# Optimization experiments

Hardware: AMD Instinct MI355X
Metric: run time of the kernel (lower is better)

## Reference

```python
import jax, jax.numpy as jnp
import numpy as np

N, E = 50000, 250000
SD, VM = 128, 64          # scalar channels, vector multiplicity (irreps: 128x0e + 64x1e)
EA, SH = 64, 4            # edge_attr dim, spherical-harmonics dim (1x0e + 1x1e)
H, FC = 16, 256
HD = FC // H              # head dim = 16
EPS = 1e-5


def _split(x):
    return x[:, :SD], x[:, SD:].reshape(-1, VM, 3)


def _ln(s, V):
    # equivariant layer norm: standardize scalars; RMS-normalize vector norms
    s = (s - s.mean(-1, keepdims=True)) * jax.lax.rsqrt(s.var(-1, keepdims=True) + EPS)
    vn = jax.lax.rsqrt(jnp.mean(jnp.sum(V * V, -1), -1, keepdims=True) + EPS)
    return s, V * vn[..., None]


def setup_inputs() -> dict:
    key = jax.random.key(0)
    ks = iter(jax.random.split(key, 48))
    rn = lambda shp, sc=1.0: jax.random.normal(next(ks), shp, dtype=jnp.float32) * sc
    w = lambda i, o: rn((i, o), 1.0 / np.sqrt(i))
    z = lambda d: jnp.zeros((d,), jnp.float32)
    return dict(
        node_features=rn((N, SD + 3 * VM)),
        edge_attr=rn((E, EA)),
        edge_sh=rn((E, SH)),
        Wq=w(SD, FC), bq=z(FC),
        Wk=w(SD, FC), bk=z(FC),
        We=w(EA, FC), be=z(FC),
        Wv_s=w(SD, SD), bv_s=z(SD), Wv_v=w(VM, VM),
        w_ss=w(SD, SD), w_vv_s=w(VM, SD), w_ssg=w(SD, VM), w_vvg=w(VM, VM),
        b_ms=z(SD), b_mg=z(VM),
        w_sv=w(SD, VM), w_vs=w(VM, VM), w_vvv=w(VM, VM),
        Wo_s=w(SD, SD), bo_s=z(SD), Wo_v=w(VM, VM),
        W1_s=w(SD, SD + VM), b1_s=z(SD + VM), W1_v=w(VM, VM),
        W2_s=w(SD, SD), b2_s=z(SD), W2_v=w(VM, VM),
        edge_index=jax.random.randint(next(ks), (2, E), 0, N, dtype=jnp.int32),
        batch=jnp.zeros((N,), jnp.int32),
    )


def reference(node_features, edge_attr, edge_sh, Wq, bq, Wk, bk, We, be,
              Wv_s, bv_s, Wv_v, w_ss, w_vv_s, w_ssg, w_vvg, b_ms, b_mg,
              w_sv, w_vs, w_vvv, Wo_s, bo_s, Wo_v,
              W1_s, b1_s, W1_v, W2_s, b2_s, W2_v, edge_index, batch):
    src, dst = edge_index[0], edge_index[1]
    ns, nV = _split(node_features)                        # [N,SD], [N,VM,3]

    # per-edge multi-head attention scores (gathered q/k + edge bias term)
    q = (ns[dst] @ Wq + bq).reshape(-1, H, HD)
    k = (ns[src] @ Wk + bk).reshape(-1, H, HD)
    ef = (edge_attr @ We + be).reshape(-1, H, HD)
    scores = ((q * k).sum(-1) + (q * ef).sum(-1)) / np.sqrt(HD)   # [E,H]

    # per-destination-node softmax (replaces the python unique(dst) loop)
    m = jax.ops.segment_max(scores, dst, num_segments=N)
    ex = jnp.exp(scores - m[dst])
    den = jax.ops.segment_sum(ex, dst, num_segments=N)
    attn = (ex / den[dst]).mean(-1, keepdims=True)                # [E,1]

    # v projection (o3.Linear) on source nodes
    vs = ns[src] @ Wv_s + bv_s                                    # [E,SD]
    Vv = jnp.einsum('evk,vu->euk', nV[src], Wv_v)                 # [E,VM,3]

    # message MLP: fully-connected tensor product with edge SH, norm, swish-gate
    shs, shv = edge_sh[:, 0], edge_sh[:, 1:4]
    s_in = vs * shs[:, None]                                      # 0e x 0e -> 0e
    dots = jnp.einsum('evk,ek->ev', Vv, shv)                      # 1e x 1e -> 0e
    ms = s_in @ w_ss + dots @ w_vv_s + b_ms                       # [E,SD] scalars
    mg = s_in @ w_ssg + dots @ w_vvg + b_mg                       # [E,VM] gates
    MV = ((vs @ w_sv)[:, :, None] * shv[:, None, :]               # 0e x 1e -> 1e
          + jnp.einsum('evk,vu->euk', Vv * shs[:, None, None], w_vs)   # 1e x 0e -> 1e
          + jnp.einsum('evk,vu->euk', jnp.cross(Vv, shv[:, None, :]), w_vvv))  # 1e x 1e -> 1e
    sg, MVn = _ln(jnp.concatenate([ms, mg], -1), MV)
    msg_s = jax.nn.silu(sg[:, :SD])
    msg_V = MVn * jax.nn.sigmoid(sg[:, SD:])[:, :, None]

    # attention-weighted scatter-sum aggregation to destination nodes
    agg_s = jax.ops.segment_sum(msg_s * attn, dst, num_segments=N)
    agg_V = jax.ops.segment_sum(msg_V * attn[:, :, None], dst, num_segments=N)

    # out projection + residual + norm1
    x_s = ns + (agg_s @ Wo_s + bo_s)
    x_V = nV + jnp.einsum('nvk,vu->nuk', agg_V, Wo_v)
    x_s, x_V = _ln(x_s, x_V)

    # gated equivariant FFN + residual + norm2
    f = x_s @ W1_s + b1_s                                         # [N,SD+VM]
    fV = jnp.einsum('nvk,vu->nuk', x_V, W1_v)
    gV = fV * jax.nn.sigmoid(f[:, SD:])[:, :, None]
    o_s = x_s + (jax.nn.silu(f[:, :SD]) @ W2_s + b2_s)
    o_V = x_V + jnp.einsum('nvk,vu->nuk', gV, W2_v)
    o_s, o_V = _ln(o_s, o_V)
    return jnp.concatenate([o_s, o_V.reshape(-1, 3 * VM)], -1)
```

## Files before the change

kernel.cpp:

```cpp
#include <hip/hip_runtime.h>
#include <hip/hip_bf16.h>

#define NNODE 50000
#define NEDGE 250000

typedef __hip_bfloat16 bf16;
typedef __attribute__((ext_vector_type(8))) short short8v;
typedef __attribute__((ext_vector_type(4))) float f32x4;

__device__ __forceinline__ float b2f(bf16 x){ return __bfloat162float(x); }
__device__ __forceinline__ bf16  f2b(float x){ return __float2bfloat16(x); }
__device__ __forceinline__ short f2s(float x){ bf16 h=f2b(x); short s; __builtin_memcpy(&s,&h,2); return s; }
__device__ __forceinline__ float s2f(short s){ bf16 h; __builtin_memcpy(&h,&s,2); return b2f(h); }
__device__ __forceinline__ float sigm(float x){ return 1.0f/(1.0f+__expf(-x)); }
__device__ __forceinline__ float wred64(float v){
  #pragma unroll
  for(int o=32;o>0;o>>=1) v+=__shfl_xor(v,o,64);
  return v;
}
__device__ __forceinline__ float gred16(float v){
  v+=__shfl_xor(v,1,64); v+=__shfl_xor(v,2,64); v+=__shfl_xor(v,4,64); v+=__shfl_xor(v,8,64);
  return v;
}
__device__ __forceinline__ int ired64(int v){
  #pragma unroll
  for(int o=32;o>0;o>>=1) v+=__shfl_xor(v,o,64);
  return v;
}
__device__ __forceinline__ int fragOff(int r, int k){
  int kt=k>>5, k32=k&31, half=k32>>4, g=(k32&15)>>2, j=k32&3;
  return (kt<<10)+((r+(g<<4))<<4)+(half<<3)+(j<<1);
}
__device__ __forceinline__ short8v pack8(float4 a, float4 b){
  short8v s; s[0]=f2s(a.x);s[1]=f2s(a.y);s[2]=f2s(a.z);s[3]=f2s(a.w);
  s[4]=f2s(b.x);s[5]=f2s(b.y);s[6]=f2s(b.z);s[7]=f2s(b.w); return s;
}
__device__ __forceinline__ short8v pack8s(short4 a, short4 b){
  short8v s; s[0]=a.x;s[1]=a.y;s[2]=a.z;s[3]=a.w;s[4]=b.x;s[5]=b.y;s[6]=b.z;s[7]=b.w; return s;
}

#define T_WOS 0
#define T_WOV 32
#define T_W1S 40
#define T_W1V 88
#define T_W2S 96
#define T_W2V 128
#define T_WE  136
#define T_WQ  168
#define T_WK  232
#define T_WVS 296
#define T_WSS 328
#define T_WSSG 360
#define T_WSV 376
#define T_WVV 392
#define T_WVVS 400
#define T_WVVG 416
#define T_WVS2 424
#define T_WVVV 432
#define T_TOT 440

__global__ __launch_bounds__(64) void k_prep(
  const float* __restrict__ Wo_s, const float* __restrict__ Wo_v,
  const float* __restrict__ W1_s, const float* __restrict__ W1_v,
  const float* __restrict__ W2_s, const float* __restrict__ W2_v,
  const float* __restrict__ WeM,
  const float* __restrict__ Wq, const float* __restrict__ Wk,
  const float* __restrict__ Wv_s,
  const float* __restrict__ w_ss, const float* __restrict__ w_ssg,
  const float* __restrict__ w_sv,
  const float* __restrict__ Wv_v, const float* __restrict__ w_vv_s,
  const float* __restrict__ w_vvg, const float* __restrict__ w_vs,
  const float* __restrict__ w_vvv,
  short* __restrict__ P)
{
  const int T=blockIdx.x, l=threadIdx.x;
  const float* W; int N, KT, lt;
  if(T<T_WOV){ W=Wo_s; N=128; KT=4; lt=T; }
  else if(T<T_W1S){ W=Wo_v; N=64; KT=2; lt=T-T_WOV; }
  else if(T<T_W1V){ W=W1_s; N=192; KT=4; lt=T-T_W1S; }
  else if(T<T_W2S){ W=W1_v; N=64; KT=2; lt=T-T_W1V; }
  else if(T<T_W2V){ W=W2_s; N=128; KT=4; lt=T-T_W2S; }
  else if(T<T_WE){ W=W2_v; N=64; KT=2; lt=T-T_W2V; }
  else if(T<T_WQ){ W=WeM; N=256; KT=2; lt=T-T_WE; }
  else if(T<T_WK){ W=Wq; N=256; KT=4; lt=T-T_WQ; }
  else if(T<T_WVS){ W=Wk; N=256; KT=4; lt=T-T_WK; }
  else if(T<T_WSS){ W=Wv_s; N=128; KT=4; lt=T-T_WVS; }
  else if(T<T_WSSG){ W=w_ss; N=128; KT=4; lt=T-T_WSS; }
  else if(T<T_WSV){ W=w_ssg; N=64; KT=4; lt=T-T_WSSG; }
  else if(T<T_WVV){ W=w_sv; N=64; KT=4; lt=T-T_WSV; }
  else if(T<T_WVVS){ W=Wv_v; N=64; KT=2; lt=T-T_WVV; }
  else if(T<T_WVVG){ W=w_vv_s; N=128; KT=2; lt=T-T_WVVS; }
  else if(T<T_WVS2){ W=w_vvg; N=64; KT=2; lt=T-T_WVVG; }
  else if(T<T_WVVV){ W=w_vs; N=64; KT=2; lt=T-T_WVS2; }
  else { W=w_vvv; N=64; KT=2; lt=T-T_WVVV; }
  const int nt=lt/KT, kt=lt-nt*KT;
  const int col=nt*16+(l&15);
  short8v o;
  #pragma unroll
  for(int j=0;j<8;j++){
    int k=kt*32+((j>>2)<<4)+((l>>4)<<2)+(j&3);
    o[j]=f2s(W[(size_t)k*N+col]);
  }
  *(short8v*)(P+((size_t)T<<9)+(l<<3))=o;
}


__global__ __launch_bounds__(256) void k1_mfma(
  const float* __restrict__ nf, const short* __restrict__ P,
  const float* __restrict__ bq, const float* __restrict__ bk,
  const float* __restrict__ bvs,
  bf16* __restrict__ Q, bf16* __restrict__ K, short* __restrict__ NREC2)
{
  __shared__ __align__(16) short nsF[4*512];
  __shared__ __align__(16) short vsF[4*512];
  const int t=threadIdx.x, l=t&63, w=t>>6;
  const int n0=blockIdx.x*16;
  for(int i=t;i<512;i+=256){
    int r=i>>5, c=(i&31)<<2;
    const float4 v=*(const float4*)&nf[(size_t)(n0+r)*320+c];
    short4 s; s.x=f2s(v.x); s.y=f2s(v.y); s.z=f2s(v.z); s.w=f2s(v.w);
    *(short4*)((char*)nsF+fragOff(r,c))=s;
  }
  __syncthreads();
  short8v a[4];
  #pragma unroll
  for(int kt=0;kt<4;kt++) a[kt]=*(const short8v*)((const char*)nsF+(kt<<10)+(l<<4));
  #pragma unroll
  for(int ii=0;ii<4;ii++){
    int nt=w+(ii<<2);
    f32x4 accq={0.f,0.f,0.f,0.f}, acck={0.f,0.f,0.f,0.f};
    #pragma unroll
    for(int kt=0;kt<4;kt++){
      short8v bq8=*(const short8v*)(P+(((size_t)(T_WQ+nt*4+kt))<<9)+(l<<3));
      short8v bk8=*(const short8v*)(P+(((size_t)(T_WK+nt*4+kt))<<9)+(l<<3));
      accq=__builtin_amdgcn_mfma_f32_16x16x32_bf16(a[kt],bq8,accq,0,0,0);
      acck=__builtin_amdgcn_mfma_f32_16x16x32_bf16(a[kt],bk8,acck,0,0,0);
    }
    int col=(nt<<4)+(l&15);
    float bqs=bq[col], bks=bk[col];
    #pragma unroll
    for(int r=0;r<4;r++){
      int row=((l>>4)<<2)+r;
      Q[(size_t)(n0+row)*256+col]=f2b(accq[r]+bqs);
      K[(size_t)(n0+row)*256+col]=f2b(acck[r]+bks);
    }
  }
  #pragma unroll
  for(int ii=0;ii<2;ii++){
    int nt=w+(ii<<2);
    f32x4 acc={0.f,0.f,0.f,0.f};
    #pragma unroll
    for(int kt=0;kt<4;kt++){
      short8v b=*(const short8v*)(P+(((size_t)(T_WVS+nt*4+kt))<<9)+(l<<3));
      acc=__builtin_amdgcn_mfma_f32_16x16x32_bf16(a[kt],b,acc,0,0,0);
    }
    int col=(nt<<4)+(l&15);
    float bv=bvs[col];
    #pragma unroll
    for(int r=0;r<4;r++){
      int row=((l>>4)<<2)+r;
      *(short*)((char*)vsF+fragOff(row,col))=f2s(acc[r]+bv);
    }
  }
  __syncthreads();
  #pragma unroll
  for(int kt=0;kt<4;kt++) a[kt]=*(const short8v*)((const char*)vsF+(kt<<10)+(l<<4));
  #pragma unroll
  for(int ii=0;ii<4;ii++){
    int nt=w+(ii<<2);
    int bt;
    if(nt<8) bt=T_WSS+nt*4;
    else if(nt<12) bt=T_WSSG+(nt-8)*4;
    else bt=T_WSV+(nt-12)*4;
    f32x4 acc={0.f,0.f,0.f,0.f};
    #pragma unroll
    for(int kt=0;kt<4;kt++){
      short8v b=*(const short8v*)(P+(((size_t)(bt+kt))<<9)+(l<<3));
      acc=__builtin_amdgcn_mfma_f32_16x16x32_bf16(a[kt],b,acc,0,0,0);
    }
    int col=(nt<<4)+(l&15);
    int lane, sslot;
    if(nt<8){ lane=col&63; sslot=(col>=64)?1:0; }
    else if(nt<12){ lane=col-128; sslot=2; }
    else { lane=col-192; sslot=3; }
    #pragma unroll
    for(int r=0;r<4;r++){
      int row=((l>>4)<<2)+r;
      NREC2[(size_t)(n0+row)*1280 + (lane<<2) + sslot]=f2s(acc[r]);
    }
  }
}

__global__ __launch_bounds__(256) void k2_mfma(
  const float* __restrict__ nf, const short* __restrict__ P,
  short* __restrict__ NREC2)
{
  __shared__ __align__(16) short nvF[6*512];
  __shared__ __align__(16) short vvF[6*512];
  const int t=threadIdx.x, l=t&63, w=t>>6;
  const int n0=blockIdx.x*16;
  for(int i=t;i<3072;i+=256){
    int r=i/192, c=i-r*192;
    int v=c/3, k=c-3*v;
    float x=nf[(size_t)(n0+r)*320+128+c];
    *(short*)((char*)nvF+(k<<11)+fragOff(r,v))=f2s(x);
  }
  __syncthreads();
  #pragma unroll
  for(int jj=0;jj<3;jj++){
    int job=w+(jj<<2);
    int p=job>>2, nt=job&3;
    f32x4 acc={0.f,0.f,0.f,0.f};
    #pragma unroll
    for(int kt=0;kt<2;kt++){
      short8v a2=*(const short8v*)((const char*)nvF+(p<<11)+(kt<<10)+(l<<4));
      short8v b=*(const short8v*)(P+(((size_t)(T_WVV+nt*2+kt))<<9)+(l<<3));
      acc=__builtin_amdgcn_mfma_f32_16x16x32_bf16(a2,b,acc,0,0,0);
    }
    int col=(nt<<4)+(l&15);
    #pragma unroll
    for(int r=0;r<4;r++){
      int row=((l>>4)<<2)+r;
      *(short*)((char*)vvF+(p<<11)+fragOff(row,col))=f2s(acc[r]);
    }
  }
  __syncthreads();
  #pragma unroll
  for(int jj=0;jj<15;jj++){
    int job=w+(jj<<2);
    int p=job/20, r20=job-p*20;
    int nt, bt, G0;
    if(r20<8){ nt=r20; bt=T_WVVS+nt*2; G0=0; }
    else if(r20<12){ nt=r20-8; bt=T_WVVG+nt*2; G0=1; }
    else if(r20<16){ nt=r20-12; bt=T_WVS2+nt*2; G0=2; }
    else { nt=r20-16; bt=T_WVVV+nt*2; G0=3; }
    f32x4 acc={0.f,0.f,0.f,0.f};
    #pragma unroll
    for(int kt=0;kt<2;kt++){
      short8v a2=*(const short8v*)((const char*)vvF+(p<<11)+(kt<<10)+(l<<4));
      short8v b=*(const short8v*)(P+(((size_t)(bt+kt))<<9)+(l<<3));
      acc=__builtin_amdgcn_mfma_f32_16x16x32_bf16(a2,b,acc,0,0,0);
    }
    int col=(nt<<4)+(l&15);
    int G;
    if(G0==0)      G = p*2 + (col>=64 ? 1 : 0);
    else if(G0==1) G = 6 + p;
    else if(G0==2) G = 9 + p;
    else           G = 12 + p;
    int lane = col & 63;
    int addr = ((1+(G>>2))<<8) + (lane<<2) + (G&3);
    #pragma unroll
    for(int r=0;r<4;r++){
      int row=((l>>4)<<2)+r;
      NREC2[(size_t)(n0+row)*1280 + addr]=f2s(acc[r]);
    }
  }
}

#define SCAN_NB 196

__global__ __launch_bounds__(256) void k_scan1(const int* __restrict__ counts, int* __restrict__ bsum){
  const int t=threadIdx.x, ln=t&63, wid=t>>6;
  int idx=blockIdx.x*256+t;
  int v=(idx<NNODE)?counts[idx]:0;
  int s=ired64(v);
  __shared__ int ws[4];
  if(ln==0) ws[wid]=s;
  __syncthreads();
  if(t==0) bsum[blockIdx.x]=ws[0]+ws[1]+ws[2]+ws[3];
}

__global__ __launch_bounds__(256) void k_scan2(const int* __restrict__ bsum, int* __restrict__ boff){
  const int t=threadIdx.x, ln=t&63, wid=t>>6;
  int v=(t<SCAN_NB)?bsum[t]:0;
  int incl=v;
  #pragma unroll
  for(int o=1;o<64;o<<=1){ int x=__shfl_up(incl,o,64); if(ln>=o) incl+=x; }
  __shared__ int wtot[4], wpre[4];
  if(ln==63) wtot[wid]=incl;
  __syncthreads();
  if(t==0){ int s=0; for(int k=0;k<4;k++){ wpre[k]=s; s+=wtot[k]; } }
  __syncthreads();
  if(t<SCAN_NB) boff[t]=wpre[wid]+incl-v;
}

__global__ __launch_bounds__(256) void k_scan3(const int* __restrict__ counts, const int* __restrict__ boff,
                                               int* __restrict__ off, int* __restrict__ cursor){
  const int t=threadIdx.x, ln=t&63, wid=t>>6;
  int idx=blockIdx.x*256+t;
  int v=(idx<NNODE)?counts[idx]:0;
  int incl=v;
  #pragma unroll
  for(int o=1;o<64;o<<=1){ int x=__shfl_up(incl,o,64); if(ln>=o) incl+=x; }
  __shared__ int wtot[4], wpre[4];
  if(ln==63) wtot[wid]=incl;
  __syncthreads();
  if(t==0){ int s=0; for(int k=0;k<4;k++){ wpre[k]=s; s+=wtot[k]; } }
  __syncthreads();
  int excl=boff[blockIdx.x]+wpre[wid]+incl-v;
  if(idx<NNODE){ off[idx]=excl; cursor[idx]=excl; }
  if(blockIdx.x==SCAN_NB-1 && t==255) off[NNODE]=NEDGE;
}

__global__ __launch_bounds__(256) void k_scatter(
  const int* __restrict__ eidx, const float* __restrict__ esh,
  int* __restrict__ cursor, int* __restrict__ eord,
  int* __restrict__ srcs, float* __restrict__ eshs)
{
  int e=blockIdx.x*256+threadIdx.x;
  if(e<NEDGE){
    int d=eidx[NEDGE+e];
    int pos=atomicAdd(&cursor[d],1);
    eord[pos]=e;
    srcs[pos]=eidx[e];
    *(float4*)&eshs[(size_t)pos*4]=*(const float4*)&esh[(size_t)e*4];
  }
}

__global__ __launch_bounds__(256) void k3_mfma(
  const float* __restrict__ eattr, const int* __restrict__ eidx,
  const short* __restrict__ P, const float* __restrict__ be,
  const bf16* __restrict__ Q, const bf16* __restrict__ K,
  float* __restrict__ SC, int* __restrict__ counts)
{
  __shared__ __align__(16) short aeF[2*512];
  __shared__ __align__(16) float ef[16][260];
  __shared__ int ssrc[16], sdst[16];
  const int t=threadIdx.x, l=t&63, w=t>>6;
  const int e0=blockIdx.x*16;
  if(t<16){
    ssrc[t]=eidx[e0+t];
    int d=eidx[NEDGE+e0+t];
    sdst[t]=d;
    atomicAdd(&counts[d],1);
  }
  {
    int r=t>>4, c4=(t&15)<<2;
    const float4 v=*(const float4*)&eattr[(size_t)(e0+r)*64+c4];
    short4 s; s.x=f2s(v.x); s.y=f2s(v.y); s.z=f2s(v.z); s.w=f2s(v.w);
    *(short4*)((char*)aeF+fragOff(r,c4))=s;
  }
  __syncthreads();
  {
    short8v a0=*(const short8v*)((const char*)aeF+(l<<4));
    short8v a1=*(const short8v*)((const char*)aeF+1024+(l<<4));
    #pragma unroll
    for(int ii=0;ii<4;ii++){
      int nt=w+(ii<<2);
      f32x4 acc={0.f,0.f,0.f,0.f};
      short8v b0=*(const short8v*)(P+(((size_t)(T_WE+nt*2+0))<<9)+(l<<3));
      short8v b1=*(const short8v*)(P+(((size_t)(T_WE+nt*2+1))<<9)+(l<<3));
      acc=__builtin_amdgcn_mfma_f32_16x16x32_bf16(a0,b0,acc,0,0,0);
      acc=__builtin_amdgcn_mfma_f32_16x16x32_bf16(a1,b1,acc,0,0,0);
      int col=(nt<<4)+(l&15);
      float bv=be[col];
      #pragma unroll
      for(int r=0;r<4;r++){ int row=((l>>4)<<2)+r; ef[row][col]=acc[r]+bv; }
    }
  }
  __syncthreads();
  {
    const int h=l&15, qt=l>>4;
    const int ch=h*16+(qt<<2);
    #pragma unroll
    for(int j=0;j<4;j++){
      int el=w*4+j;
      int s=ssrc[el], d=sdst[el];
      short4 qs=*(const short4*)((const short*)Q+(size_t)d*256+ch);
      short4 ks=*(const short4*)((const short*)K+(size_t)s*256+ch);
      const float4 e4=*(const float4*)&ef[el][ch];
      float p = s2f(qs.x)*(s2f(ks.x)+e4.x)
              + s2f(qs.y)*(s2f(ks.y)+e4.y)
              + s2f(qs.z)*(s2f(ks.z)+e4.z)
              + s2f(qs.w)*(s2f(ks.w)+e4.w);
      p += __shfl_xor(p,16,64);
      p += __shfl_xor(p,32,64);
      if(qt==0) SC[(size_t)(e0+el)*16+h]=p*0.25f;
    }
  }
}

__global__ __launch_bounds__(256) void k5_att(
  const float* __restrict__ SC, const int* __restrict__ OFF,
  const int* __restrict__ EORD, float* __restrict__ ATTs)
{
  const int l=threadIdx.x&63;
  const int n=blockIdx.x*4+(threadIdx.x>>6);
  const int beg=OFF[n], end=OFF[n+1];
  const int j=l>>4, h=l&15;
  float mh=-1e30f;
  for(int i=beg+j;i<end;i+=4) mh=fmaxf(mh, SC[(size_t)EORD[i]*16+h]);
  mh=fmaxf(mh,__shfl_xor(mh,16,64));
  mh=fmaxf(mh,__shfl_xor(mh,32,64));
  float dh=0.f;
  for(int i=beg+j;i<end;i+=4) dh+=__expf(SC[(size_t)EORD[i]*16+h]-mh);
  dh+=__shfl_xor(dh,16,64);
  dh+=__shfl_xor(dh,32,64);
  float rdh=(end>beg)?1.f/dh:0.f;
  for(int i0=beg;i0<end;i0+=4){
    int i=i0+j;
    float a=0.f; bool act=(i<end);
    if(act) a=__expf(SC[(size_t)EORD[i]*16+h]-mh)*rdh;
    a=gred16(a);
    if(h==0 && act) ATTs[i]=a*(1.f/16.f);
  }
}

__global__ __launch_bounds__(256) void k6_agg(
  const int* __restrict__ SRCs, const float* __restrict__ ESHs,
  const short* __restrict__ NREC2, const float* __restrict__ ATTs,
  const int* __restrict__ OFF,
  const float* __restrict__ b_ms, const float* __restrict__ b_mg,
  float* __restrict__ AGS, float* __restrict__ AGV)
{
  const int l = threadIdx.x & 63;
  const int n = blockIdx.x*4 + (threadIdx.x>>6);
  const int beg=OFF[n], end=OFF[n+1];
  const float bmsa=b_ms[l], bmsb=b_ms[64+l], bmgv=b_mg[l];

  float as0=0.f,as1=0.f,av0acc=0.f,av1acc=0.f,av2acc=0.f;
  for(int i=beg;i<end;i++){
    const int s=SRCs[i];
    const float att=ATTs[i];
    const float4 sh4=*(const float4*)&ESHs[(size_t)i*4];
    const float shs=sh4.x, sh0=sh4.y, sh1=sh4.z, sh2=sh4.w;

    const short* R = NREC2 + (size_t)s*1280 + (l<<2);
    const short4 q0=*(const short4*)(R);
    const short4 q1=*(const short4*)(R+256);
    const short4 q2=*(const short4*)(R+512);
    const short4 q3=*(const short4*)(R+768);
    const short4 q4=*(const short4*)(R+1024);

    float msa = shs*s2f(q0.x) + s2f(q1.x)*sh0 + s2f(q1.z)*sh1 + s2f(q2.x)*sh2 + bmsa;
    float msb = shs*s2f(q0.y) + s2f(q1.y)*sh0 + s2f(q1.w)*sh1 + s2f(q2.y)*sh2 + bmsb;
    float mgv = shs*s2f(q0.z) + s2f(q2.z)*sh0 + s2f(q2.w)*sh1 + s2f(q3.x)*sh2 + bmgv;

    float sum = wred64(msa+msb+mgv);
    float sq  = wred64(msa*msa+msb*msb+mgv*mgv);
    float mean = sum*(1.f/192.f);
    float var  = sq*(1.f/192.f) - mean*mean;
    float rs   = rsqrtf(var + 1e-5f);

    const float svv=s2f(q0.w);
    const float w0=s2f(q3.y), w1=s2f(q3.z), w2=s2f(q3.w);
    const float c0=s2f(q4.x), c1=s2f(q4.y), c2=s2f(q4.z);
    float cr0 = c1*sh2 - c2*sh1;
    float cr1 = c2*sh0 - c0*sh2;
    float cr2 = c0*sh1 - c1*sh0;
    float mv0 = svv*sh0 + shs*w0 + cr0;
    float mv1 = svv*sh1 + shs*w1 + cr1;
    float mv2 = svv*sh2 + shs*w2 + cr2;
    float vsq = wred64(mv0*mv0+mv1*mv1+mv2*mv2);
    float vn  = rsqrtf(vsq*(1.f/64.f) + 1e-5f);

    float sga=(msa-mean)*rs, sgb=(msb-mean)*rs, sgg=(mgv-mean)*rs;
    float wV = vn * sigm(sgg) * att;
    as0 += sga*sigm(sga)*att;
    as1 += sgb*sigm(sgb)*att;
    av0acc += mv0*wV;
    av1acc += mv1*wV;
    av2acc += mv2*wV;
  }
  AGS[(size_t)n*128+l]     =as0;
  AGS[(size_t)n*128+64+l]  =as1;
  AGV[(size_t)n*192+l]     =av0acc;
  AGV[(size_t)n*192+64+l]  =av1acc;
  AGV[(size_t)n*192+128+l] =av2acc;
}

__global__ __launch_bounds__(256) void k7_mfma(
  const float* __restrict__ nf,
  const float* __restrict__ AGS, const float* __restrict__ AGV,
  const short* __restrict__ P,
  const float* __restrict__ bo_s, const float* __restrict__ b1_s, const float* __restrict__ b2_s,
  float* __restrict__ out)
{
  __shared__ float xs[16][132];
  __shared__ short xvh[16][200];
  __shared__ short ffh[16][204];
  __shared__ __align__(16) short asA[4*512];
  __shared__ __align__(16) short avA[6*512];
  __shared__ float smean[16], srs[16], svn[16];
  const int t=threadIdx.x, l=t&63, w=t>>6;
  const int n0=blockIdx.x*16;
  const int lam=t&63, kt4=t>>6;
  const int fr=lam&15, fg=lam>>4;

  for(int i=t;i<2048;i+=256){ int r=i>>7,c=i&127; xs[r][c]=nf[(size_t)(n0+r)*320+c]; }
  for(int i=t;i<3072;i+=256){ int r=i/192,cc=i-r*192; int k=cc>>6,u=cc&63; xvh[r][cc]=f2s(nf[(size_t)(n0+r)*320+128+u*3+k]); }
  {
    const float* base=&AGS[(size_t)(n0+fr)*128 + (kt4<<5) + (fg<<2)];
    float4 va=*(const float4*)base, vb=*(const float4*)(base+16);
    *(short8v*)((char*)asA+(kt4<<10)+(lam<<4))=pack8(va,vb);
  }
  for(int i=t;i<384;i+=256){
    int seg=i>>6, lm=i&63, r=lm&15, g=lm>>4;
    int p=seg>>1, k2=seg&1;
    const float* base=&AGV[(size_t)(n0+r)*192 + (p<<6) + (k2<<5) + (g<<2)];
    float4 va=*(const float4*)base, vb=*(const float4*)(base+16);
    *(short8v*)((char*)avA+(seg<<10)+(lm<<4))=pack8(va,vb);
  }
  __syncthreads();

  {
    short8v a[4];
    #pragma unroll
    for(int kt=0;kt<4;kt++) a[kt]=*(const short8v*)((const char*)asA+(kt<<10)+(l<<4));
    #pragma unroll
    for(int ii=0;ii<2;ii++){
      int nt=w+(ii<<2);
      f32x4 acc={0.f,0.f,0.f,0.f};
      #pragma unroll
      for(int kt=0;kt<4;kt++){
        short8v b=*(const short8v*)(P+(((size_t)(T_WOS+nt*4+kt))<<9)+(l<<3));
        acc=__builtin_amdgcn_mfma_f32_16x16x32_bf16(a[kt],b,acc,0,0,0);
      }
      int col=(nt<<4)+(l&15);
      float bv=bo_s[col];
      #pragma unroll
      for(int r=0;r<4;r++){ int row=((l>>4)<<2)+r; xs[row][col]+=acc[r]+bv; }
    }
    #pragma unroll
    for(int ii=0;ii<3;ii++){
      int tid=w*3+ii, p=tid>>2, nt2=tid&3;
      f32x4 acc={0.f,0.f,0.f,0.f};
      #pragma unroll
      for(int kt=0;kt<2;kt++){
        short8v a2=*(const short8v*)((const char*)avA+(((p<<1)+kt)<<10)+(l<<4));
        short8v b=*(const short8v*)(P+(((size_t)(T_WOV+nt2*2+kt))<<9)+(l<<3));
        acc=__builtin_amdgcn_mfma_f32_16x16x32_bf16(a2,b,acc,0,0,0);
      }
      int col=(p<<6)+(nt2<<4)+(l&15);
      #pragma unroll
      for(int r=0;r<4;r++){
        int row=((l>>4)<<2)+r;
        float x=s2f(xvh[row][col]);
        xvh[row][col]=f2s(x+acc[r]);
      }
    }
  }
  __syncthreads();

  {
    const int nn=t>>4, g=t&15;
    float sum=0,sq=0;
    #pragma unroll
    for(int j=0;j<8;j++){ float x=xs[nn][g+16*j]; sum+=x; sq+=x*x; }
    sum=gred16(sum); sq=gred16(sq);
    float mean=sum*(1.f/128.f);
    float var=sq*(1.f/128.f)-mean*mean;
    float vsq=0;
    #pragma unroll
    for(int j=0;j<12;j++){ float x=s2f(xvh[nn][g+16*j]); vsq+=x*x; }
    vsq=gred16(vsq);
    if(g==0){ smean[nn]=mean; srs[nn]=rsqrtf(var+1e-5f); svn[nn]=rsqrtf(vsq*(1.f/64.f)+1e-5f); }
  }
  __syncthreads();

  for(int i=t;i<512;i+=256){
    int r=i>>5, c=(i&31)<<2;
    float m=smean[r], rs=srs[r];
    float4 v=*(float4*)&xs[r][c];
    v.x=(v.x-m)*rs; v.y=(v.y-m)*rs; v.z=(v.z-m)*rs; v.w=(v.w-m)*rs;
    *(float4*)&xs[r][c]=v;
  }
  for(int i=t;i<768;i+=256){
    int r=i/48, c=(i-r*48)<<2;
    float vn=svn[r];
    short4 sv4=*(short4*)&xvh[r][c];
    sv4.x=f2s(s2f(sv4.x)*vn); sv4.y=f2s(s2f(sv4.y)*vn);
    sv4.z=f2s(s2f(sv4.z)*vn); sv4.w=f2s(s2f(sv4.w)*vn);
    *(short4*)&xvh[r][c]=sv4;
  }
  __syncthreads();
  {
    float4 va=*(const float4*)&xs[fr][(kt4<<5)+(fg<<2)];
    float4 vb=*(const float4*)&xs[fr][(kt4<<5)+16+(fg<<2)];
    *(short8v*)((char*)asA+(kt4<<10)+(lam<<4))=pack8(va,vb);
  }
  for(int i=t;i<384;i+=256){
    int seg=i>>6, lm=i&63, r=lm&15, g=lm>>4;
    int p=seg>>1, k2=seg&1;
    short4 sa=*(const short4*)&xvh[r][(p<<6)+(k2<<5)+(g<<2)];
    short4 sb=*(const short4*)&xvh[r][(p<<6)+(k2<<5)+16+(g<<2)];
    *(short8v*)((char*)avA+(seg<<10)+(lm<<4))=pack8s(sa,sb);
  }
  __syncthreads();

  {
    short8v a[4];
    #pragma unroll
    for(int kt=0;kt<4;kt++) a[kt]=*(const short8v*)((const char*)asA+(kt<<10)+(l<<4));
    #pragma unroll
    for(int ii=0;ii<3;ii++){
      int nt=w+(ii<<2);
      f32x4 acc={0.f,0.f,0.f,0.f};
      #pragma unroll
      for(int kt=0;kt<4;kt++){
        short8v b=*(const short8v*)(P+(((size_t)(T_W1S+nt*4+kt))<<9)+(l<<3));
        acc=__builtin_amdgcn_mfma_f32_16x16x32_bf16(a[kt],b,acc,0,0,0);
      }
      int col=(nt<<4)+(l&15);
      float bv=b1_s[col];
      #pragma unroll
      for(int r=0;r<4;r++){ int row=((l>>4)<<2)+r; ffh[row][col]=f2s(acc[r]+bv); }
    }
  }
  __syncthreads();

  f32x4 g4acc[3];
  {
    #pragma unroll
    for(int ii=0;ii<3;ii++){
      int tid=w*3+ii, p=tid>>2, nt2=tid&3;
      f32x4 acc={0.f,0.f,0.f,0.f};
      #pragma unroll
      for(int kt=0;kt<2;kt++){
        short8v a2=*(const short8v*)((const char*)avA+(((p<<1)+kt)<<10)+(l<<4));
        short8v b=*(const short8v*)(P+(((size_t)(T_W1V+nt2*2+kt))<<9)+(l<<3));
        acc=__builtin_amdgcn_mfma_f32_16x16x32_bf16(a2,b,acc,0,0,0);
      }
      g4acc[ii]=acc;
    }
    for(int i=t;i<512;i+=256){
      int r=i>>5, c=(i&31)<<2;
      short4 sv4=*(short4*)&ffh[r][c];
      float x0=s2f(sv4.x), x1=s2f(sv4.y), x2=s2f(sv4.z), x3=s2f(sv4.w);
      sv4.x=f2s(x0*sigm(x0)); sv4.y=f2s(x1*sigm(x1)); sv4.z=f2s(x2*sigm(x2)); sv4.w=f2s(x3*sigm(x3));
      *(short4*)&ffh[r][c]=sv4;
    }
  }
  __syncthreads();

  {
    short4 sa=*(const short4*)&ffh[fr][(kt4<<5)+(fg<<2)];
    short4 sb=*(const short4*)&ffh[fr][(kt4<<5)+16+(fg<<2)];
    *(short8v*)((char*)asA+(kt4<<10)+(lam<<4))=pack8s(sa,sb);
  }
  {
    #pragma unroll
    for(int ii=0;ii<3;ii++){
      int tid=w*3+ii, nt2=tid&3;
      int uu=(nt2<<4)+(l&15);
      #pragma unroll
      for(int r=0;r<4;r++){
        int row=((l>>4)<<2)+r;
        g4acc[ii][r]*=sigm(s2f(ffh[row][128+uu]));
      }
    }
  }
  __syncthreads();

  {
    #pragma unroll
    for(int ii=0;ii<3;ii++){
      int tid=w*3+ii, p=tid>>2, nt2=tid&3;
      int uu=(nt2<<4)+(l&15);
      #pragma unroll
      for(int r=0;r<4;r++){
        int row=((l>>4)<<2)+r;
        ffh[row][(p<<6)+uu]=f2s(g4acc[ii][r]);
      }
    }
  }
  __syncthreads();
  for(int i=t;i<384;i+=256){
    int seg=i>>6, lm=i&63, r=lm&15, g=lm>>4;
    int p=seg>>1, k2=seg&1;
    short4 sa=*(const short4*)&ffh[r][(p<<6)+(k2<<5)+(g<<2)];
    short4 sb=*(const short4*)&ffh[r][(p<<6)+(k2<<5)+16+(g<<2)];
    *(short8v*)((char*)avA+(seg<<10)+(lm<<4))=pack8s(sa,sb);
  }
  __syncthreads();

  {
    short8v a[4];
    #pragma unroll
    for(int kt=0;kt<4;kt++) a[kt]=*(const short8v*)((const char*)asA+(kt<<10)+(l<<4));
    #pragma unroll
    for(int ii=0;ii<2;ii++){
      int nt=w+(ii<<2);
      f32x4 acc={0.f,0.f,0.f,0.f};
      #pragma unroll
      for(int kt=0;kt<4;kt++){
        short8v b=*(const short8v*)(P+(((size_t)(T_W2S+nt*4+kt))<<9)+(l<<3));
        acc=__builtin_amdgcn_mfma_f32_16x16x32_bf16(a[kt],b,acc,0,0,0);
      }
      int col=(nt<<4)+(l&15);
      float bv=b2_s[col];
      #pragma unroll
      for(int r=0;r<4;r++){ int row=((l>>4)<<2)+r; xs[row][col]+=acc[r]+bv; }
    }
    #pragma unroll
    for(int ii=0;ii<3;ii++){
      int tid=w*3+ii, p=tid>>2, nt2=tid&3;
      f32x4 acc={0.f,0.f,0.f,0.f};
      #pragma unroll
      for(int kt=0;kt<2;kt++){
        short8v a2=*(const short8v*)((const char*)avA+(((p<<1)+kt)<<10)+(l<<4));
        short8v b=*(const short8v*)(P+(((size_t)(T_W2V+nt2*2+kt))<<9)+(l<<3));
        acc=__builtin_amdgcn_mfma_f32_16x16x32_bf16(a2,b,acc,0,0,0);
      }
      int col=(p<<6)+(nt2<<4)+(l&15);
      #pragma unroll
      for(int r=0;r<4;r++){
        int row=((l>>4)<<2)+r;
        float x=s2f(xvh[row][col]);
        xvh[row][col]=f2s(x+acc[r]);
      }
    }
  }
  __syncthreads();

  {
    const int nn=t>>4, g=t&15;
    float sum=0,sq=0;
    #pragma unroll
    for(int j=0;j<8;j++){ float x=xs[nn][g+16*j]; sum+=x; sq+=x*x; }
    sum=gred16(sum); sq=gred16(sq);
    float mean=sum*(1.f/128.f);
    float var=sq*(1.f/128.f)-mean*mean;
    float vsq=0;
    #pragma unroll
    for(int j=0;j<12;j++){ float x=s2f(xvh[nn][g+16*j]); vsq+=x*x; }
    vsq=gred16(vsq);
    if(g==0){ smean[nn]=mean; srs[nn]=rsqrtf(var+1e-5f); svn[nn]=rsqrtf(vsq*(1.f/64.f)+1e-5f); }
  }
  __syncthreads();

  for(int i=t;i<16*320;i+=256){
    int nn=i/320, c=i-nn*320;
    float v;
    if(c<128) v=(xs[nn][c]-smean[nn])*srs[nn];
    else { int j=c-128; int u=j/3, k=j-u*3; v=s2f(xvh[nn][(k<<6)+u])*svn[nn]; }
    out[(size_t)(n0+nn)*320+c]=v;
  }
}

extern "C" void kernel_launch(void* const* d_in, const int* in_sizes, int n_in,
                              void* d_out, int out_size, void* d_ws, size_t ws_size,
                              hipStream_t stream)
{
  (void)in_sizes; (void)n_in; (void)out_size; (void)ws_size;
  const float* nf    =(const float*)d_in[0];
  const float* eattr =(const float*)d_in[1];
  const float* esh   =(const float*)d_in[2];
  const float* Wq    =(const float*)d_in[3];  const float* bq  =(const float*)d_in[4];
  const float* Wk    =(const float*)d_in[5];  const float* bk  =(const float*)d_in[6];
  const float* We    =(const float*)d_in[7];  const float* be  =(const float*)d_in[8];
  const float* Wv_s  =(const float*)d_in[9];  const float* bv_s=(const float*)d_in[10];
  const float* Wv_v  =(const float*)d_in[11];
  const float* w_ss  =(const float*)d_in[12]; const float* w_vv_s=(const float*)d_in[13];
  const float* w_ssg =(const float*)d_in[14]; const float* w_vvg =(const float*)d_in[15];
  const float* b_ms  =(const float*)d_in[16]; const float* b_mg  =(const float*)d_in[17];
  const float* w_sv  =(const float*)d_in[18]; const float* w_vs  =(const float*)d_in[19];
  const float* w_vvv =(const float*)d_in[20];
  const float* Wo_s  =(const float*)d_in[21]; const float* bo_s  =(const float*)d_in[22];
  const float* Wo_v  =(const float*)d_in[23];
  const float* W1_s  =(const float*)d_in[24]; const float* b1_s  =(const float*)d_in[25];
  const float* W1_v  =(const float*)d_in[26];
  const float* W2_s  =(const float*)d_in[27]; const float* b2_s  =(const float*)d_in[28];
  const float* W2_v  =(const float*)d_in[29];
  const int*   eidx  =(const int*)d_in[30];
  float* out=(float*)d_out;

  char* w=(char*)d_ws;
  bf16* Q    =(bf16*)w;  w+=(size_t)NNODE*256*2;
  bf16* Kb   =(bf16*)w;  w+=(size_t)NNODE*256*2;
  short* NREC2=(short*)w; w+=(size_t)NNODE*1280*2;
  float* SC  =(float*)w; w+=(size_t)NEDGE*16*4;
  float* ESHs=(float*)w; w+=(size_t)NEDGE*4*4;
  float* ATTs=(float*)w; w+=(size_t)NEDGE*4;
  float* AGS =(float*)w; w+=(size_t)NNODE*128*4;
  float* AGV =(float*)w; w+=(size_t)NNODE*192*4;
  short* P   =(short*)w; w+=(size_t)T_TOT*512*2;
  int* COUNTS=(int*)w;   w+=(size_t)NNODE*4;
  int* OFFb  =(int*)w;   w+=(size_t)(NNODE+1)*4;
  int* CURSOR=(int*)w;   w+=(size_t)NNODE*4;
  int* EORDb =(int*)w;   w+=(size_t)NEDGE*4;
  int* SRCs  =(int*)w;   w+=(size_t)NEDGE*4;
  int* BSUM  =(int*)w;   w+=(size_t)256*4;
  int* BOFF  =(int*)w;   w+=(size_t)256*4;

  hipMemsetAsync(COUNTS,0,(size_t)NNODE*4,stream);

  k_prep    <<<T_TOT,64,0,stream>>>(Wo_s,Wo_v,W1_s,W1_v,W2_s,W2_v,We,
                                    Wq,Wk,Wv_s,w_ss,w_ssg,w_sv,
                                    Wv_v,w_vv_s,w_vvg,w_vs,w_vvv,P);
  k1_mfma   <<<NNODE/16,256,0,stream>>>(nf,P,bq,bk,bv_s,Q,Kb,NREC2);
  k2_mfma   <<<NNODE/16,256,0,stream>>>(nf,P,NREC2);
  k3_mfma   <<<NEDGE/16,256,0,stream>>>(eattr,eidx,P,be,Q,Kb,SC,COUNTS);
  k_scan1   <<<SCAN_NB,256,0,stream>>>(COUNTS,BSUM);
  k_scan2   <<<1,256,0,stream>>>(BSUM,BOFF);
  k_scan3   <<<SCAN_NB,256,0,stream>>>(COUNTS,BOFF,OFFb,CURSOR);
  k_scatter <<<(NEDGE+255)/256,256,0,stream>>>(eidx,esh,CURSOR,EORDb,SRCs,ESHs);
  k5_att    <<<NNODE/4,256,0,stream>>>(SC,OFFb,EORDb,ATTs);
  k6_agg    <<<NNODE/4,256,0,stream>>>(SRCs,ESHs,NREC2,ATTs,OFFb,b_ms,b_mg,AGS,AGV);
  k7_mfma   <<<NNODE/16,256,0,stream>>>(nf,AGS,AGV,P,bo_s,b1_s,b2_s,out);
}
```

Baseline: 460.3 us.

## Compute attention scores in dst-sorted edge order to drop EORD indirection

Moves the CSR build (new histogram kernel, scan, scatter) ahead of the score kernel. k3 now processes edges in dst-sorted order and writes SC in that order, so k5 reads SC contiguously instead of through EORD. The Q gathers in k3 become mostly repeated within a block, which improves locality. In exchange, k3 gathers edge_attr through EORD, an extra launch is added, and DSTs reuses the ATTs buffer, which is safe only because k5 overwrites ATTs after k3 has consumed DSTs.

```diff
diff --git a/kernel.cpp b/kernel.cpp
--- a/kernel.cpp
+++ b/kernel.cpp
@@ -104,7 +104,6 @@
   *(short8v*)(P+((size_t)T<<9)+(l<<3))=o;
 }
 
-
 __global__ __launch_bounds__(256) void k1_mfma(
   const float* __restrict__ nf, const short* __restrict__ P,
   const float* __restrict__ bq, const float* __restrict__ bk,
@@ -257,6 +256,11 @@
   }
 }
 
+__global__ __launch_bounds__(256) void k_hist(const int* __restrict__ eidx, int* __restrict__ counts){
+  int e=blockIdx.x*256+threadIdx.x;
+  if(e<NEDGE) atomicAdd(&counts[eidx[NEDGE+e]],1);
+}
+
 #define SCAN_NB 196
 
 __global__ __launch_bounds__(256) void k_scan1(const int* __restrict__ counts, int* __restrict__ bsum){
@@ -305,7 +309,7 @@
 __global__ __launch_bounds__(256) void k_scatter(
   const int* __restrict__ eidx, const float* __restrict__ esh,
   int* __restrict__ cursor, int* __restrict__ eord,
-  int* __restrict__ srcs, float* __restrict__ eshs)
+  int* __restrict__ srcs, int* __restrict__ dsts, float* __restrict__ eshs)
 {
   int e=blockIdx.x*256+threadIdx.x;
   if(e<NEDGE){
@@ -313,30 +317,32 @@
     int pos=atomicAdd(&cursor[d],1);
     eord[pos]=e;
     srcs[pos]=eidx[e];
+    dsts[pos]=d;
     *(float4*)&eshs[(size_t)pos*4]=*(const float4*)&esh[(size_t)e*4];
   }
 }
 
 __global__ __launch_bounds__(256) void k3_mfma(
-  const float* __restrict__ eattr, const int* __restrict__ eidx,
+  const float* __restrict__ eattr,
+  const int* __restrict__ EORD, const int* __restrict__ SRCs, const int* __restrict__ DSTs,
   const short* __restrict__ P, const float* __restrict__ be,
   const bf16* __restrict__ Q, const bf16* __restrict__ K,
-  float* __restrict__ SC, int* __restrict__ counts)
+  float* __restrict__ SC)
 {
   __shared__ __align__(16) short aeF[2*512];
   __shared__ __align__(16) float ef[16][260];
-  __shared__ int ssrc[16], sdst[16];
+  __shared__ int sed[16], ssrc[16], sdst[16];
   const int t=threadIdx.x, l=t&63, w=t>>6;
   const int e0=blockIdx.x*16;
   if(t<16){
-    ssrc[t]=eidx[e0+t];
-    int d=eidx[NEDGE+e0+t];
-    sdst[t]=d;
-    atomicAdd(&counts[d],1);
-  }
+    sed[t]=EORD[e0+t];
+    ssrc[t]=SRCs[e0+t];
+    sdst[t]=DSTs[e0+t];
+  }
+  __syncthreads();
   {
     int r=t>>4, c4=(t&15)<<2;
-    const float4 v=*(const float4*)&eattr[(size_t)(e0+r)*64+c4];
+    const float4 v=*(const float4*)&eattr[(size_t)sed[r]*64+c4];
     short4 s; s.x=f2s(v.x); s.y=f2s(v.y); s.z=f2s(v.z); s.w=f2s(v.w);
     *(short4*)((char*)aeF+fragOff(r,c4))=s;
   }
@@ -382,25 +388,25 @@
 
 __global__ __launch_bounds__(256) void k5_att(
   const float* __restrict__ SC, const int* __restrict__ OFF,
-  const int* __restrict__ EORD, float* __restrict__ ATTs)
+  float* __restrict__ ATTs)
 {
   const int l=threadIdx.x&63;
   const int n=blockIdx.x*4+(threadIdx.x>>6);
   const int beg=OFF[n], end=OFF[n+1];
   const int j=l>>4, h=l&15;
   float mh=-1e30f;
-  for(int i=beg+j;i<end;i+=4) mh=fmaxf(mh, SC[(size_t)EORD[i]*16+h]);
+  for(int i=beg+j;i<end;i+=4) mh=fmaxf(mh, SC[(size_t)i*16+h]);
   mh=fmaxf(mh,__shfl_xor(mh,16,64));
   mh=fmaxf(mh,__shfl_xor(mh,32,64));
   float dh=0.f;
-  for(int i=beg+j;i<end;i+=4) dh+=__expf(SC[(size_t)EORD[i]*16+h]-mh);
+  for(int i=beg+j;i<end;i+=4) dh+=__expf(SC[(size_t)i*16+h]-mh);
   dh+=__shfl_xor(dh,16,64);
   dh+=__shfl_xor(dh,32,64);
   float rdh=(end>beg)?1.f/dh:0.f;
   for(int i0=beg;i0<end;i0+=4){
     int i=i0+j;
     float a=0.f; bool act=(i<end);
-    if(act) a=__expf(SC[(size_t)EORD[i]*16+h]-mh)*rdh;
+    if(act) a=__expf(SC[(size_t)i*16+h]-mh)*rdh;
     a=gred16(a);
     if(h==0 && act) ATTs[i]=a*(1.f/16.f);
   }
@@ -782,20 +788,22 @@
   int* SRCs  =(int*)w;   w+=(size_t)NEDGE*4;
   int* BSUM  =(int*)w;   w+=(size_t)256*4;
   int* BOFF  =(int*)w;   w+=(size_t)256*4;
+  int* DSTs = (int*)ATTs;
 
   hipMemsetAsync(COUNTS,0,(size_t)NNODE*4,stream);
 
   k_prep    <<<T_TOT,64,0,stream>>>(Wo_s,Wo_v,W1_s,W1_v,W2_s,W2_v,We,
                                     Wq,Wk,Wv_s,w_ss,w_ssg,w_sv,
                                     Wv_v,w_vv_s,w_vvg,w_vs,w_vvv,P);
-  k1_mfma   <<<NNODE/16,256,0,stream>>>(nf,P,bq,bk,bv_s,Q,Kb,NREC2);
-  k2_mfma   <<<NNODE/16,256,0,stream>>>(nf,P,NREC2);
-  k3_mfma   <<<NEDGE/16,256,0,stream>>>(eattr,eidx,P,be,Q,Kb,SC,COUNTS);
+  k_hist    <<<(NEDGE+255)/256,256,0,stream>>>(eidx,COUNTS);
   k_scan1   <<<SCAN_NB,256,0,stream>>>(COUNTS,BSUM);
   k_scan2   <<<1,256,0,stream>>>(BSUM,BOFF);
   k_scan3   <<<SCAN_NB,256,0,stream>>>(COUNTS,BOFF,OFFb,CURSOR);
-  k_scatter <<<(NEDGE+255)/256,256,0,stream>>>(eidx,esh,CURSOR,EORDb,SRCs,ESHs);
-  k5_att    <<<NNODE/4,256,0,stream>>>(SC,OFFb,EORDb,ATTs);
+  k_scatter <<<(NEDGE+255)/256,256,0,stream>>>(eidx,esh,CURSOR,EORDb,SRCs,DSTs,ESHs);
+  k1_mfma   <<<NNODE/16,256,0,stream>>>(nf,P,bq,bk,bv_s,Q,Kb,NREC2);
+  k2_mfma   <<<NNODE/16,256,0,stream>>>(nf,P,NREC2);
+  k3_mfma   <<<NEDGE/16,256,0,stream>>>(eattr,EORDb,SRCs,DSTs,P,be,Q,Kb,SC);
+  k5_att    <<<NNODE/4,256,0,stream>>>(SC,OFFb,ATTs);
   k6_agg    <<<NNODE/4,256,0,stream>>>(SRCs,ESHs,NREC2,ATTs,OFFb,b_ms,b_mg,AGS,AGV);
   k7_mfma   <<<NNODE/16,256,0,stream>>>(nf,AGS,AGV,P,bo_s,b1_s,b2_s,out);
 }
```

New measurement: 467.2 us. Within noise of the previous version (+1.5%).
